# Performance work log

Hardware: AMD Instinct MI355X
Metric: run time of the kernel (lower is better)

The kernel has to match this reference:

```python
import jax, jax.numpy as jnp
import numpy as np

NUM_CLIPS = 64
# (kernel, stride) per layer for each scale, per num_scale_layers=[16,8,8]
SCALE_SPECS = [[(1, 1)] + [(2, 1)] * 15,
               [(3, 2)] + [(2, 1)] * 7,
               [(3, 2)] + [(2, 1)] * 7]
KEEP = {0: (7, 15), 1: (3, 7), 2: (3, 5, 7)}


def _build_props():
    # replicates SparsePropMaxPool.__init__ construction of self.props
    tmp = [[1] * 16, [2] + [1] * 7, [2] + [1] * 7]
    acum, stride, props = 0, 1, []
    for scale_idx, strides in enumerate(tmp):
        for i, st in enumerate(strides):
            stride *= st
            if i in KEEP[scale_idx]:
                s = np.arange(0, NUM_CLIPS - acum - i * stride, stride)
                props.append(np.stack([s, s + acum + i * stride], -1))
        acum += stride * (len(strides) + 1)
    props = np.concatenate(props, 0)
    props[:, 1] += 1
    return props.astype(np.int64)  # [153, 2]


def _maxpool1d(x, k, s):
    if k == 1 and s == 1:
        return x
    return jax.lax.reduce_window(x, -jnp.inf, jax.lax.max,
                                 (1, 1, k), (1, 1, s), 'VALID')


def _forward(x, props):
    B, H, N = x.shape  # N == 64
    acum, stride = 0, 1
    s_parts, e_parts, feat_parts = [], [], []
    for scale in SCALE_SPECS:
        for i, (k, st) in enumerate(scale):
            stride *= st
            x = _maxpool1d(x, k, st)
            s = np.arange(0, N - acum - i * stride, stride)
            s_parts.append(s)
            e_parts.append(s + acum + i * stride)
            feat_parts.append(x)  # [B, H, len(s)]
        acum += stride * (len(scale) + 1)
    # all (s,e) diagonals are disjoint across layers -> one fused scatter
    s_all = np.concatenate(s_parts)
    e_all = np.concatenate(e_parts)
    feats = jnp.concatenate(feat_parts, axis=-1)  # [B, H, total]
    ori_map_h = jnp.zeros((B, H, N, N), x.dtype).at[:, :, s_all, e_all].set(feats)
    ori_map_mask = jnp.zeros((B, 1, N, N), x.dtype).at[:, :, s_all, e_all].set(1.0)
    p0, p1 = props[:, 0], props[:, 1] - 1
    props_h = jnp.transpose(ori_map_h[:, :, p0, p1], (0, 2, 1))  # [B, P, H]
    # faithful (no-op) write-back as in the torch source
    ori_map_h = ori_map_h.at[:, :, p0, p1].set(jnp.transpose(props_h, (0, 2, 1)))
    return props_h, ori_map_h, ori_map_mask


def setup_inputs() -> dict:
    key = jax.random.key(0)
    kx, kg = jax.random.split(key)
    x = jax.random.normal(kx, (64, 512, 64), dtype=jnp.float32)
    props = jnp.asarray(_build_props())  # [153, 2]
    props_graph = jax.random.randint(kg, (153, 153), 0, 2, dtype=jnp.int32)
    return {'x': x, 'props': props, 'props_graph': props_graph}


def reference(x, props, props_graph):
    return _forward(x, props)
```

## Files before the change

### kernel.cpp

```cpp
#include <hip/hip_runtime.h>


#define B_ 64
#define H_ 512
#define N_ 64
#define NPROP 153

__device__ __forceinline__ bool in_set(int s, int d) {
    if (d < 0) return false;
    if (d <= 15) return true;
    if (d <= 31) return (d & 1) && ((s & 1) == 0);
    return (d >= 35) && ((d & 3) == 3) && ((s & 3) == 0);
}

__global__ __launch_bounds__(128) void map_kernel(const float* __restrict__ x,
                                                  float* __restrict__ out_map) {
    const int lane = threadIdx.x;
    const int g    = lane >> 4;
    const int t    = lane & 15;
    const size_t bh = (size_t)blockIdx.x * 8 + g;

    __shared__ __align__(16) float xs[8][72];
    float4 xv = reinterpret_cast<const float4*>(x)[blockIdx.x * 128 + lane];
    *reinterpret_cast<float4*>(&xs[g][4 * t]) = xv;
    __syncthreads();

    float4* mrow = reinterpret_cast<float4*>(out_map + bh * (size_t)(N_ * N_));
    const int e0 = 4 * t;
    float vx = 0.f, vy = 0.f, vz = 0.f, vw = 0.f;
    #pragma unroll
    for (int s = N_ - 1; s >= 0; --s) {
        const float m = xs[g][s];
        vx = (s == e0 + 0) ? m : fmaxf(vx, m);
        vy = (s == e0 + 1) ? m : fmaxf(vy, m);
        vz = (s == e0 + 2) ? m : fmaxf(vz, m);
        vw = (s == e0 + 3) ? m : fmaxf(vw, m);
        float4 w;
        w.x = in_set(s, e0 + 0 - s) ? vx : 0.f;
        w.y = in_set(s, e0 + 1 - s) ? vy : 0.f;
        w.z = in_set(s, e0 + 2 - s) ? vz : 0.f;
        w.w = in_set(s, e0 + 3 - s) ? vw : 0.f;
        mrow[s * 16 + t] = w;
    }
}

__global__ __launch_bounds__(64) void props_kernel(const float* __restrict__ x,
                                                   float* __restrict__ out_props,
                                                   float* __restrict__ out_mask) {
    const int lane = threadIdx.x;
    const int b = blockIdx.x >> 3;
    const int c = blockIdx.x & 7;
    const int h = c * 64 + lane;

    const float4* xr = reinterpret_cast<const float4*>(x + ((size_t)b * H_ + h) * N_);
    float r[64];
    #pragma unroll
    for (int k = 0; k < 16; ++k) {
        float4 v = xr[k];
        r[4*k+0] = v.x; r[4*k+1] = v.y; r[4*k+2] = v.z; r[4*k+3] = v.w;
    }
    float a[63];
    #pragma unroll
    for (int i = 0; i < 63; ++i) a[i] = fmaxf(r[i], r[i+1]);
    float bb[61];
    #pragma unroll
    for (int i = 0; i < 61; ++i) bb[i] = fmaxf(a[i], a[i+2]);
    float T3[57];
    #pragma unroll
    for (int i = 0; i < 57; ++i) T3[i] = fmaxf(bb[i], bb[i+4]);

    float* po = out_props + (size_t)b * NPROP * H_ + h;
    int p = 0;
    #pragma unroll
    for (int s = 0; s < 57; ++s)
        po[(size_t)(p++) * H_] = T3[s];
    #pragma unroll
    for (int s = 0; s < 49; ++s)
        po[(size_t)(p++) * H_] = fmaxf(T3[s], T3[s + 8]);
    #pragma unroll
    for (int s = 0; s <= 40; s += 2)
        po[(size_t)(p++) * H_] = fmaxf(fmaxf(T3[s], T3[s + 8]), T3[s + 16]);
    #pragma unroll
    for (int s = 0; s <= 32; s += 2)
        po[(size_t)(p++) * H_] =
            fmaxf(fmaxf(T3[s], T3[s + 8]), fmaxf(T3[s + 16], T3[s + 24]));
    #pragma unroll
    for (int s = 0; s <= 16; s += 4) {
        float m = T3[s];
        #pragma unroll
        for (int j = 8; j <= 40; j += 8) m = fmaxf(m, T3[s + j]);
        po[(size_t)(p++) * H_] = m;
    }
    #pragma unroll
    for (int s = 0; s <= 8; s += 4) {
        float m = T3[s];
        #pragma unroll
        for (int j = 8; j <= 48; j += 8) m = fmaxf(m, T3[s + j]);
        po[(size_t)(p++) * H_] = m;
    }
    {
        float m = T3[0];
        #pragma unroll
        for (int j = 8; j <= 56; j += 8) m = fmaxf(m, T3[j]);
        po[(size_t)p * H_] = m;
    }

    if (c == 0) {
        float* mk = out_mask + (size_t)b * (N_ * N_);
        #pragma unroll
        for (int s = 0; s < N_; ++s)
            mk[s * N_ + lane] = in_set(s, lane - s) ? 1.0f : 0.0f;
    }
}

extern "C" void kernel_launch(void* const* d_in, const int* in_sizes, int n_in,
                              void* d_out, int out_size, void* d_ws, size_t ws_size,
                              hipStream_t stream) {
    const float* x = (const float*)d_in[0];
    float* out       = (float*)d_out;
    float* out_props = out;
    float* out_map   = out + (size_t)B_ * NPROP * H_;
    float* out_mask  = out_map + (size_t)B_ * H_ * N_ * N_;

    props_kernel<<<dim3(B_ * (H_ / 64)), dim3(64), 0, stream>>>(x, out_props, out_mask);
    map_kernel<<<dim3(B_ * H_ / 8), dim3(128), 0, stream>>>(x, out_map);
}
```

Baseline: 110.9 us.

## Fuse props and map kernels into one launch with split prop writes

Merges the props/mask kernel into the map kernel so a single launch runs both. Every eighth block first computes the proposal features, with its two wavefronts each writing half of the proposal rows and half of the mask rows, and then does its normal map tile. This removes one kernel launch and the serialization between the two kernels. In exchange those blocks carry extra register-heavy work, which can raise register pressure for the whole kernel and reduce occupancy.

```diff
diff --git a/kernel.cpp b/kernel.cpp
--- a/kernel.cpp
+++ b/kernel.cpp
@@ -13,15 +13,95 @@
     return (d >= 35) && ((d & 3) == 3) && ((s & 3) == 0);
 }
 
-__global__ __launch_bounds__(128) void map_kernel(const float* __restrict__ x,
-                                                  float* __restrict__ out_map) {
+__global__ __launch_bounds__(128) void fused_kernel(const float* __restrict__ x,
+                                                    float* __restrict__ out_props,
+                                                    float* __restrict__ out_map,
+                                                    float* __restrict__ out_mask) {
     const int lane = threadIdx.x;
-    const int g    = lane >> 4;
-    const int t    = lane & 15;
-    const size_t bh = (size_t)blockIdx.x * 8 + g;
+    const int bid  = blockIdx.x;
+
+    if ((bid & 7) == 0) {
+        const int b  = bid >> 6;
+        const int m  = (bid >> 3) & 7;
+        const int h  = m * 64 + (lane & 63);
+        const int q  = lane >> 6;
+
+        const float4* xr = reinterpret_cast<const float4*>(x + ((size_t)b * H_ + h) * N_);
+        float r[64];
+        #pragma unroll
+        for (int k = 0; k < 16; ++k) {
+            float4 v = xr[k];
+            r[4*k+0] = v.x; r[4*k+1] = v.y; r[4*k+2] = v.z; r[4*k+3] = v.w;
+        }
+        float a[63];
+        #pragma unroll
+        for (int i = 0; i < 63; ++i) a[i] = fmaxf(r[i], r[i+1]);
+        float bb[61];
+        #pragma unroll
+        for (int i = 0; i < 61; ++i) bb[i] = fmaxf(a[i], a[i+2]);
+        float T3[57];
+        #pragma unroll
+        for (int i = 0; i < 57; ++i) T3[i] = fmaxf(bb[i], bb[i+4]);
+
+        float* po = out_props + (size_t)b * NPROP * H_ + h;
+        if (q == 0) {
+            #pragma unroll
+            for (int s = 0; s < 57; ++s)
+                po[(size_t)s * H_] = T3[s];
+            #pragma unroll
+            for (int s = 0; s < 20; ++s)
+                po[(size_t)(57 + s) * H_] = fmaxf(T3[s], T3[s + 8]);
+        } else {
+            #pragma unroll
+            for (int s = 20; s < 49; ++s)
+                po[(size_t)(57 + s) * H_] = fmaxf(T3[s], T3[s + 8]);
+            int p = 106;
+            #pragma unroll
+            for (int s = 0; s <= 40; s += 2)
+                po[(size_t)(p++) * H_] = fmaxf(fmaxf(T3[s], T3[s + 8]), T3[s + 16]);
+            #pragma unroll
+            for (int s = 0; s <= 32; s += 2)
+                po[(size_t)(p++) * H_] =
+                    fmaxf(fmaxf(T3[s], T3[s + 8]), fmaxf(T3[s + 16], T3[s + 24]));
+            #pragma unroll
+            for (int s = 0; s <= 16; s += 4) {
+                float mx = T3[s];
+                #pragma unroll
+                for (int j = 8; j <= 40; j += 8) mx = fmaxf(mx, T3[s + j]);
+                po[(size_t)(p++) * H_] = mx;
+            }
+            #pragma unroll
+            for (int s = 0; s <= 8; s += 4) {
+                float mx = T3[s];
+                #pragma unroll
+                for (int j = 8; j <= 48; j += 8) mx = fmaxf(mx, T3[s + j]);
+                po[(size_t)(p++) * H_] = mx;
+            }
+            {
+                float mx = T3[0];
+                #pragma unroll
+                for (int j = 8; j <= 56; j += 8) mx = fmaxf(mx, T3[j]);
+                po[(size_t)p * H_] = mx;
+            }
+        }
+
+        if (m == 0) {
+            float* mk = out_mask + (size_t)b * (N_ * N_);
+            const int e = lane & 63;
+            #pragma unroll
+            for (int i = 0; i < 32; ++i) {
+                int s = 2 * i + q;
+                mk[s * N_ + e] = in_set(s, e - s) ? 1.0f : 0.0f;
+            }
+        }
+    }
+
+    const int g = lane >> 4;
+    const int t = lane & 15;
+    const size_t bh = (size_t)bid * 8 + g;
 
     __shared__ __align__(16) float xs[8][72];
-    float4 xv = reinterpret_cast<const float4*>(x)[blockIdx.x * 128 + lane];
+    float4 xv = reinterpret_cast<const float4*>(x)[bid * 128 + lane];
     *reinterpret_cast<float4*>(&xs[g][4 * t]) = xv;
     __syncthreads();
 
@@ -30,86 +110,17 @@
     float vx = 0.f, vy = 0.f, vz = 0.f, vw = 0.f;
     #pragma unroll
     for (int s = N_ - 1; s >= 0; --s) {
-        const float m = xs[g][s];
-        vx = (s == e0 + 0) ? m : fmaxf(vx, m);
-        vy = (s == e0 + 1) ? m : fmaxf(vy, m);
-        vz = (s == e0 + 2) ? m : fmaxf(vz, m);
-        vw = (s == e0 + 3) ? m : fmaxf(vw, m);
+        const float mv = xs[g][s];
+        vx = (s == e0 + 0) ? mv : fmaxf(vx, mv);
+        vy = (s == e0 + 1) ? mv : fmaxf(vy, mv);
+        vz = (s == e0 + 2) ? mv : fmaxf(vz, mv);
+        vw = (s == e0 + 3) ? mv : fmaxf(vw, mv);
         float4 w;
         w.x = in_set(s, e0 + 0 - s) ? vx : 0.f;
         w.y = in_set(s, e0 + 1 - s) ? vy : 0.f;
         w.z = in_set(s, e0 + 2 - s) ? vz : 0.f;
         w.w = in_set(s, e0 + 3 - s) ? vw : 0.f;
         mrow[s * 16 + t] = w;
-    }
-}
-
-__global__ __launch_bounds__(64) void props_kernel(const float* __restrict__ x,
-                                                   float* __restrict__ out_props,
-                                                   float* __restrict__ out_mask) {
-    const int lane = threadIdx.x;
-    const int b = blockIdx.x >> 3;
-    const int c = blockIdx.x & 7;
-    const int h = c * 64 + lane;
-
-    const float4* xr = reinterpret_cast<const float4*>(x + ((size_t)b * H_ + h) * N_);
-    float r[64];
-    #pragma unroll
-    for (int k = 0; k < 16; ++k) {
-        float4 v = xr[k];
-        r[4*k+0] = v.x; r[4*k+1] = v.y; r[4*k+2] = v.z; r[4*k+3] = v.w;
-    }
-    float a[63];
-    #pragma unroll
-    for (int i = 0; i < 63; ++i) a[i] = fmaxf(r[i], r[i+1]);
-    float bb[61];
-    #pragma unroll
-    for (int i = 0; i < 61; ++i) bb[i] = fmaxf(a[i], a[i+2]);
-    float T3[57];
-    #pragma unroll
-    for (int i = 0; i < 57; ++i) T3[i] = fmaxf(bb[i], bb[i+4]);
-
-    float* po = out_props + (size_t)b * NPROP * H_ + h;
-    int p = 0;
-    #pragma unroll
-    for (int s = 0; s < 57; ++s)
-        po[(size_t)(p++) * H_] = T3[s];
-    #pragma unroll
-    for (int s = 0; s < 49; ++s)
-        po[(size_t)(p++) * H_] = fmaxf(T3[s], T3[s + 8]);
-    #pragma unroll
-    for (int s = 0; s <= 40; s += 2)
-        po[(size_t)(p++) * H_] = fmaxf(fmaxf(T3[s], T3[s + 8]), T3[s + 16]);
-    #pragma unroll
-    for (int s = 0; s <= 32; s += 2)
-        po[(size_t)(p++) * H_] =
-            fmaxf(fmaxf(T3[s], T3[s + 8]), fmaxf(T3[s + 16], T3[s + 24]));
-    #pragma unroll
-    for (int s = 0; s <= 16; s += 4) {
-        float m = T3[s];
-        #pragma unroll
-        for (int j = 8; j <= 40; j += 8) m = fmaxf(m, T3[s + j]);
-        po[(size_t)(p++) * H_] = m;
-    }
-    #pragma unroll
-    for (int s = 0; s <= 8; s += 4) {
-        float m = T3[s];
-        #pragma unroll
-        for (int j = 8; j <= 48; j += 8) m = fmaxf(m, T3[s + j]);
-        po[(size_t)(p++) * H_] = m;
-    }
-    {
-        float m = T3[0];
-        #pragma unroll
-        for (int j = 8; j <= 56; j += 8) m = fmaxf(m, T3[j]);
-        po[(size_t)p * H_] = m;
-    }
-
-    if (c == 0) {
-        float* mk = out_mask + (size_t)b * (N_ * N_);
-        #pragma unroll
-        for (int s = 0; s < N_; ++s)
-            mk[s * N_ + lane] = in_set(s, lane - s) ? 1.0f : 0.0f;
     }
 }
 
@@ -122,6 +133,5 @@
     float* out_map   = out + (size_t)B_ * NPROP * H_;
     float* out_mask  = out_map + (size_t)B_ * H_ * N_ * N_;
 
-    props_kernel<<<dim3(B_ * (H_ / 64)), dim3(64), 0, stream>>>(x, out_props, out_mask);
-    map_kernel<<<dim3(B_ * H_ / 8), dim3(128), 0, stream>>>(x, out_map);
+    fused_kernel<<<dim3(B_ * H_ / 8), dim3(128), 0, stream>>>(x, out_props, out_map, out_mask);
 }
```

Result: slower. 120.7 us (+8.8%).
